# Kernel optimization log

Measured on AMD Instinct MI355X. Metric: run time of the kernel, lower is better.

Reference implementation:

```python
import jax, jax.numpy as jnp
import numpy as np


def _scatter_mean(x, idx, num_segments):
    # x: (J, F, C), idx: (F,) -> (J, B, C), mean over frames per segment
    s = jax.ops.segment_sum(jnp.swapaxes(x, 0, 1), idx, num_segments=num_segments)  # (B, J, C)
    cnt = jax.ops.segment_sum(jnp.ones(idx.shape, x.dtype), idx, num_segments=num_segments)  # (B,)
    cnt = jnp.maximum(cnt, 1.0)
    return jnp.swapaxes(s, 0, 1) / cnt[None, :, None]


def setup_inputs() -> dict:
    key = jax.random.key(0)
    k1, k2, k3 = jax.random.split(key, 3)
    J, F, C, B = 25, 38400, 128, 128
    x = jax.random.normal(k1, (J, F, C), dtype=jnp.float32)
    batch_index = jnp.sort(jax.random.randint(k2, (F,), 0, B))
    # xavier_normal_ for (C, C): std = sqrt(2 / (C + C))
    weight = jax.random.normal(k3, (C, C), dtype=jnp.float32) * np.float32(np.sqrt(2.0 / (C + C)))
    return {"x": x, "batch_index": batch_index, "num_segments": B, "weight": weight}


def reference(x, batch_index, num_segments, weight):
    # gc: per-segment mean -> (J, B, C) @ (C, C)
    gc = jnp.tanh(jnp.matmul(_scatter_mean(x, batch_index, num_segments), weight))  # (J, B, C)
    gc_gathered = jnp.take(gc, batch_index, axis=1)  # (J, F, C)
    gate = jax.nn.sigmoid(jnp.sum(x * gc_gathered, axis=-1, keepdims=True))  # (J, F, 1)
    return _scatter_mean(gate * x, batch_index, num_segments)  # (J, B, C)
```

## Files before the change

### kernel.cpp

```cpp
#include <hip/hip_runtime.h>
#include <math.h>


typedef float f4v __attribute__((ext_vector_type(4)));

__global__ void seg_bounds_kernel(const int* __restrict__ idx, int F, int B,
                                  int* __restrict__ seg) {
    int b = blockIdx.x * blockDim.x + threadIdx.x;
    if (b > B) return;
    int lo = 0, hi = F;
    while (lo < hi) {
        int mid = (lo + hi) >> 1;
        if (idx[mid] < b) lo = mid + 1; else hi = mid;
    }
    seg[b] = lo;
}

__global__ void __launch_bounds__(256) seg_mean_kernel(
    const float* __restrict__ x, const int* __restrict__ seg,
    int F, int B, float* __restrict__ mean) {
    const int bid = blockIdx.x;
    const int j = bid / B, b = bid - j * B;
    const int f0 = seg[b], f1 = seg[b + 1];
    const int tid = threadIdx.x;
    const int lane32 = tid & 31;
    const int row = tid >> 5;

    const f4v* __restrict__ xp =
        (const f4v*)(x + (size_t)j * F * 128) + lane32;
    f4v a0 = {0.f, 0.f, 0.f, 0.f};
    f4v a1 = {0.f, 0.f, 0.f, 0.f};
    f4v a2 = {0.f, 0.f, 0.f, 0.f};
    f4v a3 = {0.f, 0.f, 0.f, 0.f};

    int f = f0 + row;
    const f4v* p = xp + (size_t)f * 32;
    for (; f + 56 < f1; f += 64, p += 2048) {
        f4v v0 = __builtin_nontemporal_load(p);
        f4v v1 = __builtin_nontemporal_load(p + 256);
        f4v v2 = __builtin_nontemporal_load(p + 512);
        f4v v3 = __builtin_nontemporal_load(p + 768);
        f4v v4 = __builtin_nontemporal_load(p + 1024);
        f4v v5 = __builtin_nontemporal_load(p + 1280);
        f4v v6 = __builtin_nontemporal_load(p + 1536);
        f4v v7 = __builtin_nontemporal_load(p + 1792);
        a0 += v0; a1 += v1; a2 += v2; a3 += v3;
        a0 += v4; a1 += v5; a2 += v6; a3 += v7;
    }
    for (; f < f1; f += 8, p += 256) a0 += __builtin_nontemporal_load(p);
    a0 += a1; a2 += a3; a0 += a2;

    __shared__ f4v s[256];
    s[tid] = a0;
    __syncthreads();
#pragma unroll
    for (int stride = 128; stride >= 32; stride >>= 1) {
        if (tid < stride) {
            f4v m = s[tid] + s[tid + stride];
            s[tid] = m;
        }
        __syncthreads();
    }
    if (tid < 32) {
        float inv = 1.0f / fmaxf((float)(f1 - f0), 1.0f);
        f4v m = s[tid];
        ((f4v*)(mean + ((size_t)j * B + b) * 128))[tid] = m * inv;
    }
}

__global__ void gc_kernel(const float* __restrict__ mean,
                          const float* __restrict__ W,
                          float* __restrict__ gc) {
    const int r = blockIdx.x;
    const int t = threadIdx.x;
    __shared__ float srow[128];
    srow[t] = mean[(size_t)r * 128 + t];
    __syncthreads();
    float acc = 0.f;
#pragma unroll 8
    for (int k = 0; k < 128; ++k) acc = fmaf(srow[k], W[k * 128 + t], acc);
    gc[(size_t)r * 128 + t] = tanhf(acc);
}

__device__ __forceinline__ float dot4(const f4v a, const f4v b) {
    return a[0] * b[0] + a[1] * b[1] + a[2] * b[2] + a[3] * b[3];
}

__global__ void __launch_bounds__(256) gate_scatter_kernel(
    const float* __restrict__ x, const float* __restrict__ gc,
    const int* __restrict__ seg, int F, int B,
    float* __restrict__ out) {
    const int bid = blockIdx.x;
    const int j = bid / B, b = bid - j * B;
    const int f0 = seg[b], f1 = seg[b + 1];
    const int tid = threadIdx.x;
    const int lane32 = tid & 31;
    const int row = tid >> 5;

    const f4v* __restrict__ xp =
        (const f4v*)(x + (size_t)j * F * 128) + lane32;
    const f4v g = ((const f4v*)(gc + ((size_t)j * B + b) * 128))[lane32];

    f4v a0 = {0.f, 0.f, 0.f, 0.f};
    f4v a1 = {0.f, 0.f, 0.f, 0.f};

    int f = f0 + row;
    const f4v* p = xp + (size_t)f * 32;
    for (; f + 24 < f1; f += 32, p += 1024) {
        f4v v0 = __builtin_nontemporal_load(p);
        f4v v1 = __builtin_nontemporal_load(p + 256);
        f4v v2 = __builtin_nontemporal_load(p + 512);
        f4v v3 = __builtin_nontemporal_load(p + 768);
        float p0 = dot4(v0, g), p1 = dot4(v1, g),
              p2 = dot4(v2, g), p3 = dot4(v3, g);
#pragma unroll
        for (int m = 16; m >= 1; m >>= 1) {
            p0 += __shfl_xor(p0, m, 64);
            p1 += __shfl_xor(p1, m, 64);
            p2 += __shfl_xor(p2, m, 64);
            p3 += __shfl_xor(p3, m, 64);
        }
        float g0 = 1.0f / (1.0f + __expf(-p0));
        float g1 = 1.0f / (1.0f + __expf(-p1));
        float g2 = 1.0f / (1.0f + __expf(-p2));
        float g3 = 1.0f / (1.0f + __expf(-p3));
        a0 += g0 * v0 + g2 * v2;
        a1 += g1 * v1 + g3 * v3;
    }
    for (; f < f1; f += 8, p += 256) {
        f4v v = __builtin_nontemporal_load(p);
        float pp = dot4(v, g);
#pragma unroll
        for (int m = 16; m >= 1; m >>= 1) pp += __shfl_xor(pp, m, 64);
        float gg = 1.0f / (1.0f + __expf(-pp));
        a0 += gg * v;
    }
    a0 += a1;

    __shared__ f4v s[256];
    s[tid] = a0;
    __syncthreads();
#pragma unroll
    for (int stride = 128; stride >= 32; stride >>= 1) {
        if (tid < stride) {
            f4v m = s[tid] + s[tid + stride];
            s[tid] = m;
        }
        __syncthreads();
    }
    if (tid < 32) {
        float inv = 1.0f / fmaxf((float)(f1 - f0), 1.0f);
        f4v m = s[tid];
        ((f4v*)(out + ((size_t)j * B + b) * 128))[tid] = m * inv;
    }
}

extern "C" void kernel_launch(void* const* d_in, const int* in_sizes, int n_in,
                              void* d_out, int out_size, void* d_ws, size_t ws_size,
                              hipStream_t stream) {
    const float* x  = (const float*)d_in[0];
    const int* idx  = (const int*)d_in[1];
    const float* W  = (const float*)d_in[3];
    float* out      = (float*)d_out;

    const int F = in_sizes[1];
    int C = 1;
    while ((long long)C * C < (long long)in_sizes[3]) ++C;
    const int J = in_sizes[0] / (F * C);
    const int B = out_size / (J * C);

    char* ws = (char*)d_ws;
    int* seg = (int*)ws;
    size_t off = (((size_t)(B + 1) * sizeof(int)) + 255) & ~(size_t)255;
    float* mean = (float*)(ws + off);
    off += (((size_t)J * B * C * sizeof(float)) + 255) & ~(size_t)255;
    float* gcb = (float*)(ws + off);

    seg_bounds_kernel<<<(B + 1 + 255) / 256, 256, 0, stream>>>(idx, F, B, seg);
    seg_mean_kernel<<<J * B, 256, 0, stream>>>(x, seg, F, B, mean);
    gc_kernel<<<J * B, C, 0, stream>>>(mean, W, gcb);
    gate_scatter_kernel<<<J * B, 256, 0, stream>>>(x, gcb, seg, F, B, out);
}
```

Measured before the change: 690.4 us.

## Fuse mean and gc kernels and chunk joints so x is re-read from cache

Merges the segment-mean and gc matmul/tanh kernels into one kernel, which removes the intermediate mean buffer and one launch. The J dimension is split into three chunks, each running mean_gc then gate_scatter, so roughly 1/3 of x (~164MB) is touched between the two reads and may partly stay in the large last-level cache. The first pass now uses ordinary cached loads instead of nontemporal ones so the data can be kept for reuse. The cost is more kernel launches and reduced parallelism per launch.

```diff
diff --git a/kernel.cpp b/kernel.cpp
--- a/kernel.cpp
+++ b/kernel.cpp
@@ -16,11 +16,12 @@
     seg[b] = lo;
 }
 
-__global__ void __launch_bounds__(256) seg_mean_kernel(
+__global__ void __launch_bounds__(256) mean_gc_kernel(
     const float* __restrict__ x, const int* __restrict__ seg,
-    int F, int B, float* __restrict__ mean) {
+    const float* __restrict__ W, int F, int B, int jbase,
+    float* __restrict__ gc) {
     const int bid = blockIdx.x;
-    const int j = bid / B, b = bid - j * B;
+    const int j = jbase + bid / B, b = bid - (bid / B) * B;
     const int f0 = seg[b], f1 = seg[b + 1];
     const int tid = threadIdx.x;
     const int lane32 = tid & 31;
@@ -36,21 +37,22 @@
     int f = f0 + row;
     const f4v* p = xp + (size_t)f * 32;
     for (; f + 56 < f1; f += 64, p += 2048) {
-        f4v v0 = __builtin_nontemporal_load(p);
-        f4v v1 = __builtin_nontemporal_load(p + 256);
-        f4v v2 = __builtin_nontemporal_load(p + 512);
-        f4v v3 = __builtin_nontemporal_load(p + 768);
-        f4v v4 = __builtin_nontemporal_load(p + 1024);
-        f4v v5 = __builtin_nontemporal_load(p + 1280);
-        f4v v6 = __builtin_nontemporal_load(p + 1536);
-        f4v v7 = __builtin_nontemporal_load(p + 1792);
+        f4v v0 = p[0];
+        f4v v1 = p[256];
+        f4v v2 = p[512];
+        f4v v3 = p[768];
+        f4v v4 = p[1024];
+        f4v v5 = p[1280];
+        f4v v6 = p[1536];
+        f4v v7 = p[1792];
         a0 += v0; a1 += v1; a2 += v2; a3 += v3;
         a0 += v4; a1 += v5; a2 += v6; a3 += v7;
     }
-    for (; f < f1; f += 8, p += 256) a0 += __builtin_nontemporal_load(p);
+    for (; f < f1; f += 8, p += 256) a0 += p[0];
     a0 += a1; a2 += a3; a0 += a2;
 
     __shared__ f4v s[256];
+    __shared__ float srow[128];
     s[tid] = a0;
     __syncthreads();
 #pragma unroll
@@ -63,23 +65,19 @@
     }
     if (tid < 32) {
         float inv = 1.0f / fmaxf((float)(f1 - f0), 1.0f);
-        f4v m = s[tid];
-        ((f4v*)(mean + ((size_t)j * B + b) * 128))[tid] = m * inv;
+        f4v m = s[tid] * inv;
+        srow[tid * 4 + 0] = m[0];
+        srow[tid * 4 + 1] = m[1];
+        srow[tid * 4 + 2] = m[2];
+        srow[tid * 4 + 3] = m[3];
     }
-}
-
-__global__ void gc_kernel(const float* __restrict__ mean,
-                          const float* __restrict__ W,
-                          float* __restrict__ gc) {
-    const int r = blockIdx.x;
-    const int t = threadIdx.x;
-    __shared__ float srow[128];
-    srow[t] = mean[(size_t)r * 128 + t];
     __syncthreads();
-    float acc = 0.f;
+    if (tid < 128) {
+        float acc = 0.f;
 #pragma unroll 8
-    for (int k = 0; k < 128; ++k) acc = fmaf(srow[k], W[k * 128 + t], acc);
-    gc[(size_t)r * 128 + t] = tanhf(acc);
+        for (int k = 0; k < 128; ++k) acc = fmaf(srow[k], W[k * 128 + tid], acc);
+        gc[((size_t)j * B + b) * 128 + tid] = tanhf(acc);
+    }
 }
 
 __device__ __forceinline__ float dot4(const f4v a, const f4v b) {
@@ -88,10 +86,10 @@
 
 __global__ void __launch_bounds__(256) gate_scatter_kernel(
     const float* __restrict__ x, const float* __restrict__ gc,
-    const int* __restrict__ seg, int F, int B,
+    const int* __restrict__ seg, int F, int B, int jbase,
     float* __restrict__ out) {
     const int bid = blockIdx.x;
-    const int j = bid / B, b = bid - j * B;
+    const int j = jbase + bid / B, b = bid - (bid / B) * B;
     const int f0 = seg[b], f1 = seg[b + 1];
     const int tid = threadIdx.x;
     const int lane32 = tid & 31;
@@ -172,12 +170,16 @@
     char* ws = (char*)d_ws;
     int* seg = (int*)ws;
     size_t off = (((size_t)(B + 1) * sizeof(int)) + 255) & ~(size_t)255;
-    float* mean = (float*)(ws + off);
-    off += (((size_t)J * B * C * sizeof(float)) + 255) & ~(size_t)255;
     float* gcb = (float*)(ws + off);
 
     seg_bounds_kernel<<<(B + 1 + 255) / 256, 256, 0, stream>>>(idx, F, B, seg);
-    seg_mean_kernel<<<J * B, 256, 0, stream>>>(x, seg, F, B, mean);
-    gc_kernel<<<J * B, C, 0, stream>>>(mean, W, gcb);
-    gate_scatter_kernel<<<J * B, 256, 0, stream>>>(x, gcb, seg, F, B, out);
+
+    const int NCH = 3;
+    int jdone = 0;
+    for (int c = 0; c < NCH && jdone < J; ++c) {
+        int jcnt = (J - jdone + (NCH - 1 - c)) / (NCH - c);
+        mean_gc_kernel<<<jcnt * B, 256, 0, stream>>>(x, seg, W, F, B, jdone, gcb);
+        gate_scatter_kernel<<<jcnt * B, 256, 0, stream>>>(x, gcb, seg, F, B, jdone, out);
+        jdone += jcnt;
+    }
 }
```

Result: slower. 717.8 us (+4.0%).
